# Optimization experiments

Measured on AMD Instinct MI355X. Metric: run time of the kernel, lower is better.

## Reference

```python
import jax, jax.numpy as jnp
import numpy as np

L = 4000      # num identities
C = 8         # num cameras; center bank is label-major: center j -> (label j//C, cam j%C)
T = 0.07      # temperature
HARD_NEG_K = 50
LAMDA = 0.5


def setup_inputs() -> dict:
    key = jax.random.key(0)
    k1, k2, k3, k4 = jax.random.split(key, 4)
    n, d = 256, 2048
    feats = jax.random.normal(k1, (n, d), dtype=jnp.float32)
    centers = jax.random.normal(k2, (L * C, d), dtype=jnp.float32)
    centers = centers / jnp.linalg.norm(centers, axis=1, keepdims=True)  # bank is kept unit-norm
    labels = jax.random.randint(k3, (n,), 0, L, dtype=jnp.int64)
    camids = jax.random.randint(k4, (n,), 0, C, dtype=jnp.int64)
    return {"feats": feats, "centers": centers, "labels": labels, "camids": camids, "epoch": 5}


def _cap_losses(feats, centers, labels, camids):
    n = feats.shape[0]
    M = centers.shape[0]
    feats = feats / jnp.linalg.norm(feats, axis=1, keepdims=True)  # F.normalize(p=2, dim=1)
    center_labels = jnp.arange(M) // C
    center_cams = jnp.arange(M) % C

    sims = jnp.einsum('nd,md->nm', feats, centers) / T  # [n, M] scaled similarities
    own_idx = labels * C + camids                        # cam_label_index[(label, cam)]
    own = sims[jnp.arange(n), own_idx]                   # numerator logits
    exp_sims = jnp.exp(sims)                             # unit vectors => sims <= 1/T ~ 14.3, safe

    # ---- intra-camera loss: denominator over centers sharing the sample's camid ----
    cam_mask = (center_cams[None, :] == camids[:, None])
    denom_intra = jnp.sum(exp_sims * cam_mask, axis=1)
    loss_i = own - jnp.log(denom_intra)                  # log(frac_up/frac_down)
    # mean per camid, then sum over camids present in the batch, negated
    ones = jnp.ones((n,), dtype=feats.dtype)
    cam_sums = jax.ops.segment_sum(loss_i, camids, num_segments=C)
    cam_cnts = jax.ops.segment_sum(ones, camids, num_segments=C)
    loss_intra = -jnp.sum(jnp.where(cam_cnts > 0, cam_sums / jnp.maximum(cam_cnts, 1.0), 0.0))

    # ---- inter loss: same-label centers + first-K hard negatives (in bank order) ----
    lbl_mask = (center_labels[None, :] == labels[:, None])
    other = ~lbl_mask
    # torch concatenates other-label centers in label order and takes the FIRST 50 (a slice,
    # not top-k); label-major bank order makes that = first 50 other-label centers by index.
    rank = jnp.cumsum(other.astype(jnp.int32), axis=1)
    hard_mask = other & (rank <= HARD_NEG_K)
    denom_inter = jnp.sum(exp_sims * lbl_mask, axis=1) + jnp.sum(exp_sims * hard_mask, axis=1)
    loss_j = own - jnp.log(denom_inter)
    lbl_sums = jax.ops.segment_sum(loss_j, labels, num_segments=L)
    lbl_cnts = jax.ops.segment_sum(ones, labels, num_segments=L)
    loss_inter = -jnp.sum(jnp.where(lbl_cnts > 0, lbl_sums / jnp.maximum(lbl_cnts, 1.0), 0.0))

    return loss_intra, loss_inter


def reference(feats, centers, labels, camids, epoch):
    loss_intra, loss_inter = _cap_losses(feats, centers, labels, camids)
    if epoch < 5:  # epoch is a static python int
        return loss_intra
    return jnp.stack([loss_intra, LAMDA * loss_inter])
```

## Files before the change

kernel.cpp:

```cpp
#include <hip/hip_runtime.h>

typedef __attribute__((ext_vector_type(8))) __bf16 bf16x8;
typedef __attribute__((ext_vector_type(4))) float f32x4;

#define N_SAMP 256
#define DIM    2048
#define NCENT  32000
#define INV_T  14.285714285714285714f
#define NWG    250
#define NTILE  64


__global__ __launch_bounds__(256) void norm_kernel(const float* __restrict__ feats,
                                                   char* __restrict__ fnorm_pk,
                                                   float* __restrict__ d_acc) {
    int row = blockIdx.x;
    int tid = threadIdx.x;
    if (row < 16) d_acc[row * 256 + tid] = 0.f;
    const float* src = feats + (size_t)row * DIM;
    float4 v0 = reinterpret_cast<const float4*>(src)[2 * tid];
    float4 v1 = reinterpret_cast<const float4*>(src)[2 * tid + 1];
    float ss = v0.x * v0.x + v0.y * v0.y + v0.z * v0.z + v0.w * v0.w
             + v1.x * v1.x + v1.y * v1.y + v1.z * v1.z + v1.w * v1.w;
    #pragma unroll
    for (int off = 1; off < 64; off <<= 1) ss += __shfl_xor(ss, off, 64);
    __shared__ float wsum[4];
    if ((tid & 63) == 0) wsum[tid >> 6] = ss;
    __syncthreads();
    float inv = 1.0f / sqrtf(wsum[0] + wsum[1] + wsum[2] + wsum[3]);
    bf16x8 o;
    o[0] = (__bf16)(v0.x * inv); o[1] = (__bf16)(v0.y * inv);
    o[2] = (__bf16)(v0.z * inv); o[3] = (__bf16)(v0.w * inv);
    o[4] = (__bf16)(v1.x * inv); o[5] = (__bf16)(v1.y * inv);
    o[6] = (__bf16)(v1.z * inv); o[7] = (__bf16)(v1.w * inv);
    int tile = tid >> 2, ksub = tid & 3;
    int grp  = row >> 4;
    int lane = (row & 15) | (ksub << 4);
    *reinterpret_cast<bf16x8*>(fnorm_pk
        + ((size_t)tile * 16 + grp) * 1024 + lane * 16) = o;
}

__global__ __launch_bounds__(512, 2) void sims_kernel(
    const char* __restrict__ fnorm_pk, const float* __restrict__ centers,
    const int* __restrict__ labels, const int* __restrict__ camids,
    float* __restrict__ d_acc, float* __restrict__ d_own)
{
    __shared__ __align__(16) char sB[2][8192];

    const int tid  = threadIdx.x;
    const int wave = tid >> 6;
    const int lane = tid & 63;
    const int l15  = lane & 15;
    const int lhi  = lane >> 4;

    const int nb    = blockIdx.x;
    const int cbase = nb * 128;

    const int wr = (wave >> 1) * 64;
    const int wc = (wave & 1) * 64;

    f32x4 acc[4][4] = {};

    const float4* bsrc = reinterpret_cast<const float4*>(centers);
    const char*   apk  = fnorm_pk + ((size_t)(wave >> 1) * 4) * 1024 + lane * 16;

    const int bP = tid >> 3, bs = tid & 7;
    const int bu = bs ^ (bP & 7);
    const int brow = 2 * bP + (bu >> 2);
    const int bc8  = bu & 3;
    const size_t bbase = (size_t)(cbase + brow) * 512 + bc8 * 2;

    auto issueB = [&](int T, float4& f0, float4& f1) {
        f0 = bsrc[bbase + T * 8];
        f1 = bsrc[bbase + T * 8 + 1];
    };
    auto wrbufB = [&](int buf, const float4& f0, const float4& f1) {
        bf16x8 o;
        o[0] = (__bf16)f0.x; o[1] = (__bf16)f0.y; o[2] = (__bf16)f0.z; o[3] = (__bf16)f0.w;
        o[4] = (__bf16)f1.x; o[5] = (__bf16)f1.y; o[6] = (__bf16)f1.z; o[7] = (__bf16)f1.w;
        *reinterpret_cast<bf16x8*>(&sB[buf][tid * 16]) = o;
    };
    auto issueA = [&](int T, bf16x8 (&af)[4]) {
        const char* p = apk + (size_t)T * 16384;
        af[0] = *reinterpret_cast<const bf16x8*>(p);
        af[1] = *reinterpret_cast<const bf16x8*>(p + 1024);
        af[2] = *reinterpret_cast<const bf16x8*>(p + 2048);
        af[3] = *reinterpret_cast<const bf16x8*>(p + 3072);
    };
    auto compute = [&](int buf, const bf16x8 (&af)[4]) {
        bf16x8 bf[4];
        #pragma unroll
        for (int ni = 0; ni < 4; ++ni) {
            int row = wc + ni * 16 + l15, pair = row >> 1;
            int slot = (((row & 1) << 2) | lhi) ^ (pair & 7);
            bf[ni] = *reinterpret_cast<const bf16x8*>(&sB[buf][pair * 128 + slot * 16]);
        }
        #pragma unroll
        for (int mi = 0; mi < 4; ++mi)
            #pragma unroll
            for (int ni = 0; ni < 4; ++ni)
                acc[mi][ni] = __builtin_amdgcn_mfma_f32_16x16x32_bf16(
                    af[mi], bf[ni], acc[mi][ni], 0, 0, 0);
    };
    #define BAR() do { asm volatile("s_waitcnt lgkmcnt(0)" ::: "memory"); \
                       __builtin_amdgcn_s_barrier(); } while (0)

    float4 b0S0, b1S0, b0S1, b1S1;
    bf16x8 afA[4], afB[4];

    issueB(0, b0S0, b1S0);
    issueB(1, b0S1, b1S1);
    issueA(0, afA);
    wrbufB(0, b0S0, b1S0);
    BAR();
    for (int t = 0; t < NTILE; t += 2) {
        if (t + 2 < NTILE) issueB(t + 2, b0S0, b1S0);
        issueA(t + 1, afB);
        compute(0, afA);
        wrbufB(1, b0S1, b1S1);
        BAR();
        if (t + 3 < NTILE) issueB(t + 3, b0S1, b1S1);
        if (t + 2 < NTILE) issueA(t + 2, afA);
        compute(1, afB);
        if (t + 2 < NTILE) {
            wrbufB(0, b0S0, b1S0);
            BAR();
        }
    }

    float* slot_acc = d_acc + (nb & 7) * 512;
    #pragma unroll
    for (int mi = 0; mi < 4; ++mi) {
        #pragma unroll
        for (int r = 0; r < 4; ++r) {
            int i   = wr + mi * 16 + lhi * 4 + r;
            int lab = labels[i], cam = camids[i];
            int oidx = lab * 8 + cam;
            float pi = 0.f, pj = 0.f;
            #pragma unroll
            for (int ni = 0; ni < 4; ++ni) {
                int c = cbase + wc + ni * 16 + l15;
                float s = acc[mi][ni][r] * INV_T;
                float e = __expf(s);
                if ((l15 & 7) == cam) pi += e;
                bool ol = ((c >> 3) == lab);
                bool hard = (!ol) && (c < ((c < lab * 8) ? 50 : 58));
                if (ol || hard) pj += e;
                if (c == oidx) d_own[i] = s;
            }
            #pragma unroll
            for (int off = 1; off < 16; off <<= 1) {
                pi += __shfl_xor(pi, off, 64);
                pj += __shfl_xor(pj, off, 64);
            }
            if (l15 == 0) {
                atomicAdd(&slot_acc[i], pi);
                atomicAdd(&slot_acc[N_SAMP + i], pj);
            }
        }
    }
}

__global__ __launch_bounds__(256) void finalize_kernel(
    const float* __restrict__ d_acc, const float* __restrict__ d_own,
    const int* __restrict__ labels, const int* __restrict__ camids,
    float* __restrict__ out, int out_size)
{
    __shared__ int s_lab[N_SAMP], s_cam[N_SAMP];
    __shared__ float wsum[8];
    int tid = threadIdx.x;
    s_lab[tid] = labels[tid];
    s_cam[tid] = camids[tid];
    __syncthreads();
    int myl = s_lab[tid], myc = s_cam[tid];
    int nl = 0, nc = 0;
    for (int j = 0; j < N_SAMP; ++j) {
        nl += (s_lab[j] == myl);
        nc += (s_cam[j] == myc);
    }
    float di = 0.f, dj = 0.f;
    #pragma unroll
    for (int s = 0; s < 8; ++s) {
        di += d_acc[s * 512 + tid];
        dj += d_acc[s * 512 + 256 + tid];
    }
    float own = d_own[tid];
    float li = own - logf(di);
    float lj = own - logf(dj);
    float a = li / (float)nc;
    float b = lj / (float)nl;
    #pragma unroll
    for (int off = 1; off < 64; off <<= 1) {
        a += __shfl_xor(a, off, 64);
        b += __shfl_xor(b, off, 64);
    }
    if ((tid & 63) == 0) { wsum[tid >> 6] = a; wsum[4 + (tid >> 6)] = b; }
    __syncthreads();
    if (tid == 0) {
        float sa = wsum[0] + wsum[1] + wsum[2] + wsum[3];
        float sb = wsum[4] + wsum[5] + wsum[6] + wsum[7];
        out[0] = -sa;
        if (out_size > 1) out[1] = -0.5f * sb;
    }
}

extern "C" void kernel_launch(void* const* d_in, const int* in_sizes, int n_in,
                              void* d_out, int out_size, void* d_ws, size_t ws_size,
                              hipStream_t stream) {
    const float* feats   = (const float*)d_in[0];
    const float* centers = (const float*)d_in[1];
    const int*   labels  = (const int*)d_in[2];
    const int*   camids  = (const int*)d_in[3];
    float* out = (float*)d_out;

    char*  fnorm_pk = (char*)d_ws;
    float* d_acc    = (float*)((char*)d_ws + (size_t)1048576);
    float* d_own    = d_acc + 8 * 2 * N_SAMP;

    norm_kernel<<<N_SAMP, 256, 0, stream>>>(feats, fnorm_pk, d_acc);
    sims_kernel<<<NWG, 512, 0, stream>>>(fnorm_pk, centers, labels, camids, d_acc, d_own);
    finalize_kernel<<<1, 256, 0, stream>>>(d_acc, d_own, labels, camids, out, out_size);
}
```

Measured before the change: 89.55 us.

## Drop LDS staging; load centers directly into MFMA registers with smaller tiles

The sims kernel no longer stages center tiles through double-buffered shared memory with barriers. Each 256-thread block now handles 64 centers and all 256 samples. Every wave loads its B fragments straight from global memory in MFMA layout, converts them to bf16 in registers, and runs 500 blocks instead of 250. This removes LDS traffic and barrier synchronization, and aims for more blocks in flight. The cost is that each wave rereads the same center rows, which are no longer shared through LDS. The strided per-lane global loads are also less coalesced, and there is no explicit software prefetch.

```diff
diff --git a/kernel.cpp b/kernel.cpp
--- a/kernel.cpp
+++ b/kernel.cpp
@@ -7,7 +7,7 @@
 #define DIM    2048
 #define NCENT  32000
 #define INV_T  14.285714285714285714f
-#define NWG    250
+#define NWG    500
 #define NTILE  64
 
 
@@ -40,13 +40,11 @@
         + ((size_t)tile * 16 + grp) * 1024 + lane * 16) = o;
 }
 
-__global__ __launch_bounds__(512, 2) void sims_kernel(
+__global__ __launch_bounds__(256, 3) void sims_kernel(
     const char* __restrict__ fnorm_pk, const float* __restrict__ centers,
     const int* __restrict__ labels, const int* __restrict__ camids,
     float* __restrict__ d_acc, float* __restrict__ d_own)
 {
-    __shared__ __align__(16) char sB[2][8192];
-
     const int tid  = threadIdx.x;
     const int wave = tid >> 6;
     const int lane = tid & 63;
@@ -54,77 +52,49 @@
     const int lhi  = lane >> 4;
 
     const int nb    = blockIdx.x;
-    const int cbase = nb * 128;
-
-    const int wr = (wave >> 1) * 64;
-    const int wc = (wave & 1) * 64;
+    const int cbase = nb * 64;
 
     f32x4 acc[4][4] = {};
 
-    const float4* bsrc = reinterpret_cast<const float4*>(centers);
-    const char*   apk  = fnorm_pk + ((size_t)(wave >> 1) * 4) * 1024 + lane * 16;
+    const char* apk = fnorm_pk + (size_t)wave * 4096 + lane * 16;
+    const float* bp0 = centers + (size_t)(cbase + 0 * 16 + l15) * DIM + lhi * 8;
+    const float* bp1 = centers + (size_t)(cbase + 1 * 16 + l15) * DIM + lhi * 8;
+    const float* bp2 = centers + (size_t)(cbase + 2 * 16 + l15) * DIM + lhi * 8;
+    const float* bp3 = centers + (size_t)(cbase + 3 * 16 + l15) * DIM + lhi * 8;
 
-    const int bP = tid >> 3, bs = tid & 7;
-    const int bu = bs ^ (bP & 7);
-    const int brow = 2 * bP + (bu >> 2);
-    const int bc8  = bu & 3;
-    const size_t bbase = (size_t)(cbase + brow) * 512 + bc8 * 2;
+    #pragma unroll 2
+    for (int t = 0; t < NTILE; ++t) {
+        bf16x8 af0 = *reinterpret_cast<const bf16x8*>(apk + (size_t)t * 16384);
+        bf16x8 af1 = *reinterpret_cast<const bf16x8*>(apk + (size_t)t * 16384 + 1024);
+        bf16x8 af2 = *reinterpret_cast<const bf16x8*>(apk + (size_t)t * 16384 + 2048);
+        bf16x8 af3 = *reinterpret_cast<const bf16x8*>(apk + (size_t)t * 16384 + 3072);
 
-    auto issueB = [&](int T, float4& f0, float4& f1) {
-        f0 = bsrc[bbase + T * 8];
-        f1 = bsrc[bbase + T * 8 + 1];
-    };
-    auto wrbufB = [&](int buf, const float4& f0, const float4& f1) {
-        bf16x8 o;
-        o[0] = (__bf16)f0.x; o[1] = (__bf16)f0.y; o[2] = (__bf16)f0.z; o[3] = (__bf16)f0.w;
-        o[4] = (__bf16)f1.x; o[5] = (__bf16)f1.y; o[6] = (__bf16)f1.z; o[7] = (__bf16)f1.w;
-        *reinterpret_cast<bf16x8*>(&sB[buf][tid * 16]) = o;
-    };
-    auto issueA = [&](int T, bf16x8 (&af)[4]) {
-        const char* p = apk + (size_t)T * 16384;
-        af[0] = *reinterpret_cast<const bf16x8*>(p);
-        af[1] = *reinterpret_cast<const bf16x8*>(p + 1024);
-        af[2] = *reinterpret_cast<const bf16x8*>(p + 2048);
-        af[3] = *reinterpret_cast<const bf16x8*>(p + 3072);
-    };
-    auto compute = [&](int buf, const bf16x8 (&af)[4]) {
-        bf16x8 bf[4];
+        float4 x0 = *reinterpret_cast<const float4*>(bp0 + t * 32);
+        float4 y0 = *reinterpret_cast<const float4*>(bp0 + t * 32 + 4);
+        float4 x1 = *reinterpret_cast<const float4*>(bp1 + t * 32);
+        float4 y1 = *reinterpret_cast<const float4*>(bp1 + t * 32 + 4);
+        float4 x2 = *reinterpret_cast<const float4*>(bp2 + t * 32);
+        float4 y2 = *reinterpret_cast<const float4*>(bp2 + t * 32 + 4);
+        float4 x3 = *reinterpret_cast<const float4*>(bp3 + t * 32);
+        float4 y3 = *reinterpret_cast<const float4*>(bp3 + t * 32 + 4);
+
+        bf16x8 bf0, bf1, bf2, bf3;
+        bf0[0] = (__bf16)x0.x; bf0[1] = (__bf16)x0.y; bf0[2] = (__bf16)x0.z; bf0[3] = (__bf16)x0.w;
+        bf0[4] = (__bf16)y0.x; bf0[5] = (__bf16)y0.y; bf0[6] = (__bf16)y0.z; bf0[7] = (__bf16)y0.w;
+        bf1[0] = (__bf16)x1.x; bf1[1] = (__bf16)x1.y; bf1[2] = (__bf16)x1.z; bf1[3] = (__bf16)x1.w;
+        bf1[4] = (__bf16)y1.x; bf1[5] = (__bf16)y1.y; bf1[6] = (__bf16)y1.z; bf1[7] = (__bf16)y1.w;
+        bf2[0] = (__bf16)x2.x; bf2[1] = (__bf16)x2.y; bf2[2] = (__bf16)x2.z; bf2[3] = (__bf16)x2.w;
+        bf2[4] = (__bf16)y2.x; bf2[5] = (__bf16)y2.y; bf2[6] = (__bf16)y2.z; bf2[7] = (__bf16)y2.w;
+        bf3[0] = (__bf16)x3.x; bf3[1] = (__bf16)x3.y; bf3[2] = (__bf16)x3.z; bf3[3] = (__bf16)x3.w;
+        bf3[4] = (__bf16)y3.x; bf3[5] = (__bf16)y3.y; bf3[6] = (__bf16)y3.z; bf3[7] = (__bf16)y3.w;
+
         #pragma unroll
-        for (int ni = 0; ni < 4; ++ni) {
-            int row = wc + ni * 16 + l15, pair = row >> 1;
-            int slot = (((row & 1) << 2) | lhi) ^ (pair & 7);
-            bf[ni] = *reinterpret_cast<const bf16x8*>(&sB[buf][pair * 128 + slot * 16]);
-        }
-        #pragma unroll
-        for (int mi = 0; mi < 4; ++mi)
-            #pragma unroll
-            for (int ni = 0; ni < 4; ++ni)
-                acc[mi][ni] = __builtin_amdgcn_mfma_f32_16x16x32_bf16(
-                    af[mi], bf[ni], acc[mi][ni], 0, 0, 0);
-    };
-    #define BAR() do { asm volatile("s_waitcnt lgkmcnt(0)" ::: "memory"); \
-                       __builtin_amdgcn_s_barrier(); } while (0)
-
-    float4 b0S0, b1S0, b0S1, b1S1;
-    bf16x8 afA[4], afB[4];
-
-    issueB(0, b0S0, b1S0);
-    issueB(1, b0S1, b1S1);
-    issueA(0, afA);
-    wrbufB(0, b0S0, b1S0);
-    BAR();
-    for (int t = 0; t < NTILE; t += 2) {
-        if (t + 2 < NTILE) issueB(t + 2, b0S0, b1S0);
-        issueA(t + 1, afB);
-        compute(0, afA);
-        wrbufB(1, b0S1, b1S1);
-        BAR();
-        if (t + 3 < NTILE) issueB(t + 3, b0S1, b1S1);
-        if (t + 2 < NTILE) issueA(t + 2, afA);
-        compute(1, afB);
-        if (t + 2 < NTILE) {
-            wrbufB(0, b0S0, b1S0);
-            BAR();
+        for (int mi = 0; mi < 4; ++mi) {
+            bf16x8 af = mi == 0 ? af0 : mi == 1 ? af1 : mi == 2 ? af2 : af3;
+            acc[mi][0] = __builtin_amdgcn_mfma_f32_16x16x32_bf16(af, bf0, acc[mi][0], 0, 0, 0);
+            acc[mi][1] = __builtin_amdgcn_mfma_f32_16x16x32_bf16(af, bf1, acc[mi][1], 0, 0, 0);
+            acc[mi][2] = __builtin_amdgcn_mfma_f32_16x16x32_bf16(af, bf2, acc[mi][2], 0, 0, 0);
+            acc[mi][3] = __builtin_amdgcn_mfma_f32_16x16x32_bf16(af, bf3, acc[mi][3], 0, 0, 0);
         }
     }
 
@@ -133,13 +103,13 @@
     for (int mi = 0; mi < 4; ++mi) {
         #pragma unroll
         for (int r = 0; r < 4; ++r) {
-            int i   = wr + mi * 16 + lhi * 4 + r;
+            int i   = wave * 64 + mi * 16 + lhi * 4 + r;
             int lab = labels[i], cam = camids[i];
             int oidx = lab * 8 + cam;
             float pi = 0.f, pj = 0.f;
             #pragma unroll
             for (int ni = 0; ni < 4; ++ni) {
-                int c = cbase + wc + ni * 16 + l15;
+                int c = cbase + ni * 16 + l15;
                 float s = acc[mi][ni][r] * INV_T;
                 float e = __expf(s);
                 if ((l15 & 7) == cam) pi += e;
@@ -218,6 +188,6 @@
     float* d_own    = d_acc + 8 * 2 * N_SAMP;
 
     norm_kernel<<<N_SAMP, 256, 0, stream>>>(feats, fnorm_pk, d_acc);
-    sims_kernel<<<NWG, 512, 0, stream>>>(fnorm_pk, centers, labels, camids, d_acc, d_own);
+    sims_kernel<<<NWG, 256, 0, stream>>>(fnorm_pk, centers, labels, camids, d_acc, d_own);
     finalize_kernel<<<1, 256, 0, stream>>>(d_acc, d_own, labels, camids, out, out_size);
 }
```

Result: slower. 219.3 us (+144.9%).
